# Kernel optimization log

Hardware: AMD Instinct MI355X
Metric: run time of the kernel (lower is better)

## Reference

```python
import jax, jax.numpy as jnp
import numpy as np

EMBED_DIM = 1024
NUM_HEADS = 16
HEAD_DIM = EMBED_DIM // NUM_HEADS


def setup_inputs() -> dict:
    key = jax.random.key(0)
    kx, kw1, kb1, kw2, kb2 = jax.random.split(key, 5)
    B, T, C = 4, 2048, EMBED_DIM
    s = 1.0 / np.sqrt(C)
    return {
        "x": jax.random.normal(kx, (B, T, C), dtype=jnp.float32),
        "qkv_w": jax.random.uniform(kw1, (3 * C, C), jnp.float32, -s, s),
        "qkv_b": jax.random.uniform(kb1, (3 * C,), jnp.float32, -s, s),
        "out_w": jax.random.uniform(kw2, (C, C), jnp.float32, -s, s),
        "out_b": jax.random.uniform(kb2, (C,), jnp.float32, -s, s),
    }


def reference(x, qkv_w, qkv_b, out_w, out_b):
    B, T, C = x.shape
    H, D = NUM_HEADS, HEAD_DIM
    qkv = x @ qkv_w.T + qkv_b                      # [B,T,3C]
    qkv = qkv.reshape(B, T, 3, H, D)
    q = qkv[:, :, 0].transpose(0, 2, 1, 3)         # [B,H,T,D]
    k = qkv[:, :, 1].transpose(0, 2, 1, 3)
    v = qkv[:, :, 2].transpose(0, 2, 1, 3)
    att = jnp.einsum("bhqd,bhkd->bhqk", q, k) / jnp.sqrt(jnp.float32(D))
    causal = jnp.tril(jnp.ones((T, T), dtype=bool))
    att = jnp.where(causal, att, -jnp.inf)
    att = jax.nn.softmax(att, axis=-1)
    out = jnp.einsum("bhqk,bhkd->bhqd", att, v)    # [B,H,T,D]
    out = out.transpose(0, 2, 1, 3).reshape(B, T, C)
    return out @ out_w.T + out_b
```

## Files before the change

kernel.cpp:

```cpp
#include <hip/hip_runtime.h>
#include <stdint.h>

typedef _Float16 f16;
typedef _Float16 f16x4 __attribute__((ext_vector_type(4)));
typedef _Float16 f16x8 __attribute__((ext_vector_type(8)));
typedef float f32x4 __attribute__((ext_vector_type(4)));

#define LOG2E 1.44269504088896340736f

__device__ __forceinline__ f32x4 mfma_16x16x32(f16x8 a, f16x8 b, f32x4 c) {
    return __builtin_amdgcn_mfma_f32_16x16x32_f16(a, b, c, 0, 0, 0);
}

__device__ __forceinline__ void gload_lds16(const void* g, void* l) {
    __builtin_amdgcn_global_load_lds(
        (const __attribute__((address_space(1))) unsigned int*)g,
        (__attribute__((address_space(3))) unsigned int*)l, 16, 0, 0);
}

__global__ void cast_f32_f16(const float* __restrict__ src, f16* __restrict__ dst, int n4) {
    int i = blockIdx.x * 256 + threadIdx.x;
    if (i >= n4) return;
    float4 v = reinterpret_cast<const float4*>(src)[i];
    f16x4 o;
    o[0] = (f16)v.x; o[1] = (f16)v.y; o[2] = (f16)v.z; o[3] = (f16)v.w;
    reinterpret_cast<f16x4*>(dst)[i] = o;
}

template<int MODE>
__global__ __launch_bounds__(256, 2)
void gemm_tn(const f16* __restrict__ A, const f16* __restrict__ W,
             const float* __restrict__ bias, void* __restrict__ outp,
             int M, int N, int K)
{
    __shared__ __align__(16) f16 As[128 * 32];
    __shared__ __align__(16) f16 Bs[128 * 32];

    const int lane = threadIdx.x & 63;
    const int wave = threadIdx.x >> 6;
    const int l15 = lane & 15, l4 = lane >> 4;
    const int row0 = blockIdx.y * 128;
    const int col0 = blockIdx.x * 128;
    const int wr = wave >> 1, wc = wave & 1;

    f32x4 acc[4][4] = {};

    const int srow = lane >> 2;
    const int scol = (lane & 3) * 8;

    for (int k0 = 0; k0 < K; k0 += 32) {
        __syncthreads();
        #pragma unroll
        for (int it = 0; it < 2; ++it) {
            int chunk = it * 4 + wave;
            const f16* gA = A + (size_t)(row0 + chunk * 16 + srow) * K + k0 + scol;
            gload_lds16(gA, As + chunk * 512);
            const f16* gB = W + (size_t)(col0 + chunk * 16 + srow) * K + k0 + scol;
            gload_lds16(gB, Bs + chunk * 512);
        }
        __syncthreads();

        f16x8 af[4], bf[4];
        #pragma unroll
        for (int m = 0; m < 4; ++m)
            af[m] = *reinterpret_cast<const f16x8*>(As + (wr * 64 + m * 16 + l15) * 32 + l4 * 8);
        #pragma unroll
        for (int n = 0; n < 4; ++n)
            bf[n] = *reinterpret_cast<const f16x8*>(Bs + (wc * 64 + n * 16 + l15) * 32 + l4 * 8);
        #pragma unroll
        for (int m = 0; m < 4; ++m)
            #pragma unroll
            for (int n = 0; n < 4; ++n)
                acc[m][n] = mfma_16x16x32(af[m], bf[n], acc[m][n]);
    }

    if (MODE == 0) {
        f16* qb = (f16*)outp;
        const size_t HS = (size_t)64 * 2048 * 64;
        #pragma unroll
        for (int m = 0; m < 4; ++m) {
            int rbase = row0 + wr * 64 + m * 16 + l4 * 4;
            #pragma unroll
            for (int n = 0; n < 4; ++n) {
                int j = col0 + wc * 64 + n * 16 + l15;
                int which = j >> 10;
                int h = (j >> 6) & 15;
                int d = j & 63;
                float bj = bias[j];
                f16* base = qb + (size_t)which * HS;
                float scale = (which == 0) ? (0.125f * LOG2E) : 1.0f;
                #pragma unroll
                for (int r = 0; r < 4; ++r) {
                    int row = rbase + r;
                    int b = row >> 11, t = row & 2047;
                    size_t off = ((size_t)(b * 16 + h) * 2048 + t) * 64 + d;
                    base[off] = (f16)((acc[m][n][r] + bj) * scale);
                }
            }
        }
    } else {
        float* O = (float*)outp;
        #pragma unroll
        for (int m = 0; m < 4; ++m) {
            int rbase = row0 + wr * 64 + m * 16 + l4 * 4;
            #pragma unroll
            for (int n = 0; n < 4; ++n) {
                int j = col0 + wc * 64 + n * 16 + l15;
                float bj = bias[j];
                #pragma unroll
                for (int r = 0; r < 4; ++r)
                    O[(size_t)(rbase + r) * N + j] = acc[m][n][r] + bj;
            }
        }
    }
}

__global__ __launch_bounds__(256, 2)
void attn_kernel(const f16* __restrict__ qb, const f16* __restrict__ kb,
                 const f16* __restrict__ vb, f16* __restrict__ ob)
{
    __shared__ __align__(16) f16 Ks[64 * 64];
    __shared__ __align__(16) f16 Vs[64][72];
    __shared__ __align__(16) f16 Ps[4][16][72];

    const int bh = blockIdx.x;
    const int qblk = (int)gridDim.y - 1 - (int)blockIdx.y;
    const int lane = threadIdx.x & 63;
    const int wave = threadIdx.x >> 6;
    const int l15 = lane & 15, l4 = lane >> 4;
    const int q0 = qblk * 64;

    const f16* Qp = qb + ((size_t)bh * 2048 + q0 + wave * 16) * 64;
    f16x8 aq[2];
    aq[0] = *reinterpret_cast<const f16x8*>(Qp + l15 * 64 + l4 * 8);
    aq[1] = *reinterpret_cast<const f16x8*>(Qp + l15 * 64 + 32 + l4 * 8);

    float Mr = -1e30f, Lr = 0.0f;
    f32x4 oacc[4] = {};

    for (int kv0 = 0; kv0 <= q0; kv0 += 64) {
        __syncthreads();

        const f16* Kt = kb + ((size_t)bh * 2048 + kv0) * 64;
        #pragma unroll
        for (int it = 0; it < 2; ++it) {
            int c = it * 4 + wave;
            int p = c * 1024 + lane * 16;
            int krow = p >> 7;
            int col16 = (p >> 4) & 7;
            int s16 = col16 ^ (krow & 7);
            gload_lds16(Kt + krow * 64 + s16 * 8, Ks + c * 512);
        }
        const f16* Vt = vb + ((size_t)bh * 2048 + kv0) * 64;
        {
            const int d0 = wave * 16;
            #pragma unroll
            for (int it = 0; it < 2; ++it) {
                f16x8 v = *reinterpret_cast<const f16x8*>(Vt + lane * 64 + d0 + it * 8);
                #pragma unroll
                for (int e = 0; e < 8; ++e)
                    Vs[d0 + it * 8 + e][lane] = v[e];
            }
        }
        __syncthreads();

        const bool diag = (kv0 == q0);

        f32x4 s[4];
        #pragma unroll
        for (int n = 0; n < 4; ++n) {
            int key = n * 16 + l15;
            int cs = key & 7;
            f32x4 c = {};
            #pragma unroll
            for (int kc = 0; kc < 2; ++kc) {
                f16x8 kf = *reinterpret_cast<const f16x8*>(Ks + key * 64 + (((kc * 4 + l4) ^ cs) * 8));
                c = mfma_16x16x32(kf, aq[kc], c);
            }
            s[n] = c;
        }

        if (diag) {
            #pragma unroll
            for (int n = 0; n < 4; ++n)
                #pragma unroll
                for (int r = 0; r < 4; ++r)
                    if (n * 16 + l4 * 4 + r > wave * 16 + l15) s[n][r] = -1e30f;
        }

        float mx = -1e30f;
        #pragma unroll
        for (int n = 0; n < 4; ++n)
            #pragma unroll
            for (int r = 0; r < 4; ++r)
                mx = fmaxf(mx, s[n][r]);
        mx = fmaxf(mx, __shfl_xor(mx, 16));
        mx = fmaxf(mx, __shfl_xor(mx, 32));
        float nm = fmaxf(Mr, mx);
        float alpha = exp2f(Mr - nm);
        Mr = nm;

        float rs = 0.0f;
        #pragma unroll
        for (int n = 0; n < 4; ++n) {
            f16x4 pk;
            #pragma unroll
            for (int r = 0; r < 4; ++r) {
                float pv = exp2f(s[n][r] - nm);
                rs += pv;
                pk[r] = (f16)pv;
            }
            *reinterpret_cast<f16x4*>(&Ps[wave][l15][n * 16 + l4 * 4]) = pk;
        }
        rs += __shfl_xor(rs, 16);
        rs += __shfl_xor(rs, 32);
        Lr = Lr * alpha + rs;

        float ar[4];
        #pragma unroll
        for (int r = 0; r < 4; ++r) ar[r] = __shfl(alpha, l4 * 4 + r);
        #pragma unroll
        for (int dt = 0; dt < 4; ++dt) {
            oacc[dt][0] *= ar[0]; oacc[dt][1] *= ar[1];
            oacc[dt][2] *= ar[2]; oacc[dt][3] *= ar[3];
        }

        f16x8 pa0 = *reinterpret_cast<const f16x8*>(&Ps[wave][l15][l4 * 8]);
        f16x8 pa1 = *reinterpret_cast<const f16x8*>(&Ps[wave][l15][32 + l4 * 8]);
        #pragma unroll
        for (int dt = 0; dt < 4; ++dt) {
            int d = dt * 16 + l15;
            f16x8 v0 = *reinterpret_cast<const f16x8*>(&Vs[d][l4 * 8]);
            f16x8 v1 = *reinterpret_cast<const f16x8*>(&Vs[d][32 + l4 * 8]);
            oacc[dt] = mfma_16x16x32(pa0, v0, oacc[dt]);
            oacc[dt] = mfma_16x16x32(pa1, v1, oacc[dt]);
        }
    }

    float lr[4];
    #pragma unroll
    for (int r = 0; r < 4; ++r) lr[r] = __shfl(Lr, l4 * 4 + r);

    const int b = bh >> 4, h = bh & 15;
    f16* O = ob + ((size_t)b * 2048 + q0 + wave * 16) * 1024 + h * 64;
    #pragma unroll
    for (int dt = 0; dt < 4; ++dt) {
        int d = dt * 16 + l15;
        #pragma unroll
        for (int r = 0; r < 4; ++r)
            O[(size_t)(l4 * 4 + r) * 1024 + d] = (f16)(oacc[dt][r] / lr[r]);
    }
}

extern "C" void kernel_launch(void* const* d_in, const int* in_sizes, int n_in,
                              void* d_out, int out_size, void* d_ws, size_t ws_size,
                              hipStream_t stream)
{
    const float* x    = (const float*)d_in[0];
    const float* qkvw = (const float*)d_in[1];
    const float* qkvb = (const float*)d_in[2];
    const float* outw = (const float*)d_in[3];
    const float* outb = (const float*)d_in[4];
    float* out = (float*)d_out;

    f16* x_h    = (f16*)d_ws;
    f16* qkvw_h = x_h + (size_t)8192 * 1024;
    f16* outw_h = qkvw_h + (size_t)3072 * 1024;
    f16* q_buf  = outw_h + (size_t)1024 * 1024;
    f16* att_o  = q_buf + (size_t)3 * 8388608;

    cast_f32_f16<<<8192, 256, 0, stream>>>(x, x_h, 2097152);
    cast_f32_f16<<<3072, 256, 0, stream>>>(qkvw, qkvw_h, 786432);
    cast_f32_f16<<<1024, 256, 0, stream>>>(outw, outw_h, 262144);

    gemm_tn<0><<<dim3(24, 64), 256, 0, stream>>>(x_h, qkvw_h, qkvb, q_buf, 8192, 3072, 1024);
    attn_kernel<<<dim3(64, 32), 256, 0, stream>>>(q_buf, q_buf + 8388608, q_buf + 2 * 8388608, att_o);
    gemm_tn<1><<<dim3(8, 64), 256, 0, stream>>>(att_o, outw_h, outb, out, 8192, 1024, 1024);
}
```

Baseline: 202.2 us.

## Enlarge attention query tile, cache K/V fragments, remap GEMM workgroups across XCDs

The attention kernel now gives each block 128 queries (32 per wave, two 16-row groups), so each K/V tile loaded into LDS is reused twice as much. K and V fragments are held in registers for both groups, and MFMA sections are wrapped in s_setprio. Softmax probabilities are packed to f16 with cvt_pkrtz. The GEMM remaps workgroup IDs so consecutive tiles land on the same XCD for L2 locality, and attention launch bounds move to 3 waves/SIMD. The extra register pressure from the held fragments may conflict with the higher occupancy target, and the round-toward-zero conversion changes rounding slightly.

```diff
diff --git a/kernel.cpp b/kernel.cpp
--- a/kernel.cpp
+++ b/kernel.cpp
@@ -2,6 +2,7 @@
 #include <stdint.h>
 
 typedef _Float16 f16;
+typedef _Float16 f16x2 __attribute__((ext_vector_type(2)));
 typedef _Float16 f16x4 __attribute__((ext_vector_type(4)));
 typedef _Float16 f16x8 __attribute__((ext_vector_type(8)));
 typedef float f32x4 __attribute__((ext_vector_type(4)));
@@ -16,6 +17,10 @@
     __builtin_amdgcn_global_load_lds(
         (const __attribute__((address_space(1))) unsigned int*)g,
         (__attribute__((address_space(3))) unsigned int*)l, 16, 0, 0);
+}
+
+__device__ __forceinline__ f16x2 cvt_pk_f16(float a, float b) {
+    return __builtin_bit_cast(f16x2, __builtin_amdgcn_cvt_pkrtz(a, b));
 }
 
 __global__ void cast_f32_f16(const float* __restrict__ src, f16* __restrict__ dst, int n4) {
@@ -39,8 +44,13 @@
     const int lane = threadIdx.x & 63;
     const int wave = threadIdx.x >> 6;
     const int l15 = lane & 15, l4 = lane >> 4;
-    const int row0 = blockIdx.y * 128;
-    const int col0 = blockIdx.x * 128;
+
+    const int nwg = (int)(gridDim.x * gridDim.y);
+    int orig = (int)(blockIdx.y * gridDim.x + blockIdx.x);
+    int cpx = nwg >> 3;
+    int w = (orig & 7) * cpx + (orig >> 3);
+    const int row0 = (w / (int)gridDim.x) * 128;
+    const int col0 = (w % (int)gridDim.x) * 128;
     const int wr = wave >> 1, wc = wave & 1;
 
     f32x4 acc[4][4] = {};
@@ -115,7 +125,7 @@
     }
 }
 
-__global__ __launch_bounds__(256, 2)
+__global__ __launch_bounds__(256, 3)
 void attn_kernel(const f16* __restrict__ qb, const f16* __restrict__ kb,
                  const f16* __restrict__ vb, f16* __restrict__ ob)
 {
@@ -123,132 +133,155 @@
     __shared__ __align__(16) f16 Vs[64][72];
     __shared__ __align__(16) f16 Ps[4][16][72];
 
-    const int bh = blockIdx.x;
+    const int tid = (int)threadIdx.x;
+    const int bh = (int)blockIdx.x;
     const int qblk = (int)gridDim.y - 1 - (int)blockIdx.y;
-    const int lane = threadIdx.x & 63;
-    const int wave = threadIdx.x >> 6;
+    const int lane = tid & 63;
+    const int wave = tid >> 6;
     const int l15 = lane & 15, l4 = lane >> 4;
-    const int q0 = qblk * 64;
-
-    const f16* Qp = qb + ((size_t)bh * 2048 + q0 + wave * 16) * 64;
-    f16x8 aq[2];
-    aq[0] = *reinterpret_cast<const f16x8*>(Qp + l15 * 64 + l4 * 8);
-    aq[1] = *reinterpret_cast<const f16x8*>(Qp + l15 * 64 + 32 + l4 * 8);
-
-    float Mr = -1e30f, Lr = 0.0f;
-    f32x4 oacc[4] = {};
-
-    for (int kv0 = 0; kv0 <= q0; kv0 += 64) {
+    const int q0 = qblk * 128;
+    const int qw = q0 + wave * 32;
+
+    const f16* Qp = qb + ((size_t)bh * 2048 + qw) * 64;
+    f16x8 aq[2][2];
+    #pragma unroll
+    for (int g = 0; g < 2; ++g)
+        #pragma unroll
+        for (int kc = 0; kc < 2; ++kc)
+            aq[g][kc] = *reinterpret_cast<const f16x8*>(Qp + (g * 16 + l15) * 64 + kc * 32 + l4 * 8);
+
+    float Mr[2] = {-1e30f, -1e30f}, Lr[2] = {0.0f, 0.0f};
+    f32x4 oacc[2][4] = {};
+
+    const int ntiles = q0 / 64 + 2;
+
+    for (int t = 0; t < ntiles; ++t) {
+        const int kv0 = t * 64;
         __syncthreads();
 
         const f16* Kt = kb + ((size_t)bh * 2048 + kv0) * 64;
         #pragma unroll
         for (int it = 0; it < 2; ++it) {
-            int c = it * 4 + wave;
-            int p = c * 1024 + lane * 16;
-            int krow = p >> 7;
-            int col16 = (p >> 4) & 7;
-            int s16 = col16 ^ (krow & 7);
-            gload_lds16(Kt + krow * 64 + s16 * 8, Ks + c * 512);
+            int c = it * 256 + tid;
+            int krow = c >> 3;
+            int s16 = (c & 7) ^ (krow & 7);
+            gload_lds16(Kt + krow * 64 + s16 * 8, Ks + it * 2048 + wave * 512);
         }
         const f16* Vt = vb + ((size_t)bh * 2048 + kv0) * 64;
-        {
-            const int d0 = wave * 16;
-            #pragma unroll
-            for (int it = 0; it < 2; ++it) {
-                f16x8 v = *reinterpret_cast<const f16x8*>(Vt + lane * 64 + d0 + it * 8);
-                #pragma unroll
-                for (int e = 0; e < 8; ++e)
-                    Vs[d0 + it * 8 + e][lane] = v[e];
-            }
+        #pragma unroll
+        for (int it = 0; it < 2; ++it) {
+            int dblk = wave * 2 + it;
+            f16x8 v = *reinterpret_cast<const f16x8*>(Vt + lane * 64 + dblk * 8);
+            #pragma unroll
+            for (int e = 0; e < 8; ++e)
+                Vs[dblk * 8 + e][lane] = v[e];
         }
         __syncthreads();
 
-        const bool diag = (kv0 == q0);
-
-        f32x4 s[4];
+        f16x8 kf[4][2], vf[4][2];
         #pragma unroll
         for (int n = 0; n < 4; ++n) {
             int key = n * 16 + l15;
-            int cs = key & 7;
-            f32x4 c = {};
-            #pragma unroll
-            for (int kc = 0; kc < 2; ++kc) {
-                f16x8 kf = *reinterpret_cast<const f16x8*>(Ks + key * 64 + (((kc * 4 + l4) ^ cs) * 8));
-                c = mfma_16x16x32(kf, aq[kc], c);
-            }
-            s[n] = c;
-        }
-
-        if (diag) {
+            #pragma unroll
+            for (int kc = 0; kc < 2; ++kc)
+                kf[n][kc] = *reinterpret_cast<const f16x8*>(Ks + key * 64 + (((kc * 4 + l4) ^ (key & 7)) * 8));
+        }
+        #pragma unroll
+        for (int dt = 0; dt < 4; ++dt) {
+            int d = dt * 16 + l15;
+            #pragma unroll
+            for (int kc = 0; kc < 2; ++kc)
+                vf[dt][kc] = *reinterpret_cast<const f16x8*>(&Vs[d][kc * 32 + l4 * 8]);
+        }
+
+        #pragma unroll
+        for (int g = 0; g < 2; ++g) {
+            const int qbase = qw + g * 16;
+            if (kv0 > qbase + 15) continue;
+
+            f32x4 s[4];
+            __builtin_amdgcn_s_setprio(1);
+            #pragma unroll
+            for (int n = 0; n < 4; ++n) {
+                f32x4 c = {};
+                c = mfma_16x16x32(kf[n][0], aq[g][0], c);
+                c = mfma_16x16x32(kf[n][1], aq[g][1], c);
+                s[n] = c;
+            }
+            __builtin_amdgcn_s_setprio(0);
+
+            if (kv0 + 63 > qbase) {
+                #pragma unroll
+                for (int n = 0; n < 4; ++n)
+                    #pragma unroll
+                    for (int r = 0; r < 4; ++r)
+                        if (kv0 + n * 16 + l4 * 4 + r > qbase + l15) s[n][r] = -1e30f;
+            }
+
+            float mx = -1e30f;
             #pragma unroll
             for (int n = 0; n < 4; ++n)
                 #pragma unroll
                 for (int r = 0; r < 4; ++r)
-                    if (n * 16 + l4 * 4 + r > wave * 16 + l15) s[n][r] = -1e30f;
-        }
-
-        float mx = -1e30f;
-        #pragma unroll
-        for (int n = 0; n < 4; ++n)
-            #pragma unroll
-            for (int r = 0; r < 4; ++r)
-                mx = fmaxf(mx, s[n][r]);
-        mx = fmaxf(mx, __shfl_xor(mx, 16));
-        mx = fmaxf(mx, __shfl_xor(mx, 32));
-        float nm = fmaxf(Mr, mx);
-        float alpha = exp2f(Mr - nm);
-        Mr = nm;
-
-        float rs = 0.0f;
-        #pragma unroll
-        for (int n = 0; n < 4; ++n) {
-            f16x4 pk;
-            #pragma unroll
-            for (int r = 0; r < 4; ++r) {
-                float pv = exp2f(s[n][r] - nm);
-                rs += pv;
-                pk[r] = (f16)pv;
-            }
-            *reinterpret_cast<f16x4*>(&Ps[wave][l15][n * 16 + l4 * 4]) = pk;
-        }
-        rs += __shfl_xor(rs, 16);
-        rs += __shfl_xor(rs, 32);
-        Lr = Lr * alpha + rs;
-
-        float ar[4];
-        #pragma unroll
-        for (int r = 0; r < 4; ++r) ar[r] = __shfl(alpha, l4 * 4 + r);
-        #pragma unroll
-        for (int dt = 0; dt < 4; ++dt) {
-            oacc[dt][0] *= ar[0]; oacc[dt][1] *= ar[1];
-            oacc[dt][2] *= ar[2]; oacc[dt][3] *= ar[3];
-        }
-
-        f16x8 pa0 = *reinterpret_cast<const f16x8*>(&Ps[wave][l15][l4 * 8]);
-        f16x8 pa1 = *reinterpret_cast<const f16x8*>(&Ps[wave][l15][32 + l4 * 8]);
+                    mx = fmaxf(mx, s[n][r]);
+            mx = fmaxf(mx, __shfl_xor(mx, 16));
+            mx = fmaxf(mx, __shfl_xor(mx, 32));
+            float nm = fmaxf(Mr[g], mx);
+            float alpha = exp2f(Mr[g] - nm);
+            Mr[g] = nm;
+
+            float rs = 0.0f;
+            #pragma unroll
+            for (int n = 0; n < 4; ++n) {
+                float p0 = exp2f(s[n][0] - nm);
+                float p1 = exp2f(s[n][1] - nm);
+                float p2 = exp2f(s[n][2] - nm);
+                float p3 = exp2f(s[n][3] - nm);
+                rs += (p0 + p1) + (p2 + p3);
+                f16x2 lo = cvt_pk_f16(p0, p1);
+                f16x2 hi = cvt_pk_f16(p2, p3);
+                f16x4 pk; pk[0] = lo[0]; pk[1] = lo[1]; pk[2] = hi[0]; pk[3] = hi[1];
+                *reinterpret_cast<f16x4*>(&Ps[wave][l15][n * 16 + l4 * 4]) = pk;
+            }
+            rs += __shfl_xor(rs, 16);
+            rs += __shfl_xor(rs, 32);
+            Lr[g] = Lr[g] * alpha + rs;
+
+            float ar[4];
+            #pragma unroll
+            for (int r = 0; r < 4; ++r) ar[r] = __shfl(alpha, l4 * 4 + r);
+            #pragma unroll
+            for (int dt = 0; dt < 4; ++dt) {
+                oacc[g][dt][0] *= ar[0]; oacc[g][dt][1] *= ar[1];
+                oacc[g][dt][2] *= ar[2]; oacc[g][dt][3] *= ar[3];
+            }
+
+            f16x8 pa0 = *reinterpret_cast<const f16x8*>(&Ps[wave][l15][l4 * 8]);
+            f16x8 pa1 = *reinterpret_cast<const f16x8*>(&Ps[wave][l15][32 + l4 * 8]);
+            __builtin_amdgcn_s_setprio(1);
+            #pragma unroll
+            for (int dt = 0; dt < 4; ++dt) {
+                oacc[g][dt] = mfma_16x16x32(pa0, vf[dt][0], oacc[g][dt]);
+                oacc[g][dt] = mfma_16x16x32(pa1, vf[dt][1], oacc[g][dt]);
+            }
+            __builtin_amdgcn_s_setprio(0);
+        }
+    }
+
+    const int b = bh >> 4, h = bh & 15;
+    #pragma unroll
+    for (int g = 0; g < 2; ++g) {
+        float lr[4];
+        #pragma unroll
+        for (int r = 0; r < 4; ++r) lr[r] = __shfl(Lr[g], l4 * 4 + r);
+        f16* O = ob + ((size_t)b * 2048 + qw + g * 16) * 1024 + h * 64;
         #pragma unroll
         for (int dt = 0; dt < 4; ++dt) {
             int d = dt * 16 + l15;
-            f16x8 v0 = *reinterpret_cast<const f16x8*>(&Vs[d][l4 * 8]);
-            f16x8 v1 = *reinterpret_cast<const f16x8*>(&Vs[d][32 + l4 * 8]);
-            oacc[dt] = mfma_16x16x32(pa0, v0, oacc[dt]);
-            oacc[dt] = mfma_16x16x32(pa1, v1, oacc[dt]);
-        }
-    }
-
-    float lr[4];
-    #pragma unroll
-    for (int r = 0; r < 4; ++r) lr[r] = __shfl(Lr, l4 * 4 + r);
-
-    const int b = bh >> 4, h = bh & 15;
-    f16* O = ob + ((size_t)b * 2048 + q0 + wave * 16) * 1024 + h * 64;
-    #pragma unroll
-    for (int dt = 0; dt < 4; ++dt) {
-        int d = dt * 16 + l15;
-        #pragma unroll
-        for (int r = 0; r < 4; ++r)
-            O[(size_t)(l4 * 4 + r) * 1024 + d] = (f16)(oacc[dt][r] / lr[r]);
+            #pragma unroll
+            for (int r = 0; r < 4; ++r)
+                O[(size_t)(l4 * 4 + r) * 1024 + d] = (f16)(oacc[g][dt][r] / lr[r]);
+        }
     }
 }
 
@@ -274,6 +307,6 @@
     cast_f32_f16<<<1024, 256, 0, stream>>>(outw, outw_h, 262144);
 
     gemm_tn<0><<<dim3(24, 64), 256, 0, stream>>>(x_h, qkvw_h, qkvb, q_buf, 8192, 3072, 1024);
-    attn_kernel<<<dim3(64, 32), 256, 0, stream>>>(q_buf, q_buf + 8388608, q_buf + 2 * 8388608, att_o);
+    attn_kernel<<<dim3(64, 16), 256, 0, stream>>>(q_buf, q_buf + 8388608, q_buf + 2 * 8388608, att_o);
     gemm_tn<1><<<dim3(8, 64), 256, 0, stream>>>(att_o, outw_h, outb, out, 8192, 1024, 1024);
 }
```

After: 197.4 us. -2.4%, faster.

## Double-buffer attention K/V tiles, add lazy rescale and XCD-aware GEMM tile remap

Applied to the files above, without the earlier changes.

The attention kernel now double-buffers K and V in LDS, prefetching the next tile's K with global-to-LDS loads and V into registers while the current tile computes, so only one barrier is needed per iteration. It also skips the online-softmax rescale unless the running max grows by more than a threshold, uses packed f16 conversion, raises MFMA wave priority, and bumps launch_bounds occupancy to 3. Separately, the GEMM remaps workgroup IDs so neighbouring tiles land on the same XCD for better L2 reuse. The costs are higher LDS use per block and reliance on the bounded-growth threshold for the accuracy of exp values.

```diff
diff --git a/kernel.cpp b/kernel.cpp
--- a/kernel.cpp
+++ b/kernel.cpp
@@ -2,6 +2,7 @@
 #include <stdint.h>
 
 typedef _Float16 f16;
+typedef _Float16 f16x2 __attribute__((ext_vector_type(2)));
 typedef _Float16 f16x4 __attribute__((ext_vector_type(4)));
 typedef _Float16 f16x8 __attribute__((ext_vector_type(8)));
 typedef float f32x4 __attribute__((ext_vector_type(4)));
@@ -16,6 +17,10 @@
     __builtin_amdgcn_global_load_lds(
         (const __attribute__((address_space(1))) unsigned int*)g,
         (__attribute__((address_space(3))) unsigned int*)l, 16, 0, 0);
+}
+
+__device__ __forceinline__ f16x2 cvt_pk_f16(float a, float b) {
+    return __builtin_bit_cast(f16x2, __builtin_amdgcn_cvt_pkrtz(a, b));
 }
 
 __global__ void cast_f32_f16(const float* __restrict__ src, f16* __restrict__ dst, int n4) {
@@ -39,8 +44,13 @@
     const int lane = threadIdx.x & 63;
     const int wave = threadIdx.x >> 6;
     const int l15 = lane & 15, l4 = lane >> 4;
-    const int row0 = blockIdx.y * 128;
-    const int col0 = blockIdx.x * 128;
+
+    const int nwg = (int)(gridDim.x * gridDim.y);
+    int orig = (int)(blockIdx.y * gridDim.x + blockIdx.x);
+    int cpx = nwg >> 3;
+    int w = (orig & 7) * cpx + (orig >> 3);
+    const int row0 = (w / (int)gridDim.x) * 128;
+    const int col0 = (w % (int)gridDim.x) * 128;
     const int wr = wave >> 1, wc = wave & 1;
 
     f32x4 acc[4][4] = {};
@@ -115,72 +125,92 @@
     }
 }
 
-__global__ __launch_bounds__(256, 2)
+__global__ __launch_bounds__(256, 3)
 void attn_kernel(const f16* __restrict__ qb, const f16* __restrict__ kb,
                  const f16* __restrict__ vb, f16* __restrict__ ob)
 {
-    __shared__ __align__(16) f16 Ks[64 * 64];
-    __shared__ __align__(16) f16 Vs[64][72];
+    __shared__ __align__(16) f16 Ks[2][64 * 64];
+    __shared__ __align__(16) f16 Vs[2][64][72];
     __shared__ __align__(16) f16 Ps[4][16][72];
 
-    const int bh = blockIdx.x;
+    const int tid = (int)threadIdx.x;
+    const int bh = (int)blockIdx.x;
     const int qblk = (int)gridDim.y - 1 - (int)blockIdx.y;
-    const int lane = threadIdx.x & 63;
-    const int wave = threadIdx.x >> 6;
+    const int lane = tid & 63;
+    const int wave = tid >> 6;
     const int l15 = lane & 15, l4 = lane >> 4;
     const int q0 = qblk * 64;
-
-    const f16* Qp = qb + ((size_t)bh * 2048 + q0 + wave * 16) * 64;
-    f16x8 aq[2];
-    aq[0] = *reinterpret_cast<const f16x8*>(Qp + l15 * 64 + l4 * 8);
-    aq[1] = *reinterpret_cast<const f16x8*>(Qp + l15 * 64 + 32 + l4 * 8);
+    const int qw = q0 + wave * 16;
+
+    const f16* Qp = qb + ((size_t)bh * 2048 + qw) * 64;
+    f16x8 aq0 = *reinterpret_cast<const f16x8*>(Qp + l15 * 64 + l4 * 8);
+    f16x8 aq1 = *reinterpret_cast<const f16x8*>(Qp + l15 * 64 + 32 + l4 * 8);
 
     float Mr = -1e30f, Lr = 0.0f;
     f32x4 oacc[4] = {};
 
-    for (int kv0 = 0; kv0 <= q0; kv0 += 64) {
+    const int ntiles = q0 / 64 + 1;
+    const f16* Kbh = kb + (size_t)bh * 2048 * 64;
+    const f16* Vbh = vb + (size_t)bh * 2048 * 64;
+
+    f16x8 vld0, vld1;
+    {
+        #pragma unroll
+        for (int it = 0; it < 2; ++it) {
+            int c = it * 256 + tid;
+            int krow = c >> 3;
+            int s16 = (c & 7) ^ (krow & 7);
+            gload_lds16(Kbh + krow * 64 + s16 * 8, &Ks[0][0] + it * 2048 + wave * 512);
+        }
+        vld0 = *reinterpret_cast<const f16x8*>(Vbh + lane * 64 + (wave * 2 + 0) * 8);
+        vld1 = *reinterpret_cast<const f16x8*>(Vbh + lane * 64 + (wave * 2 + 1) * 8);
+    }
+
+    for (int t = 0; t < ntiles; ++t) {
+        const int cur = t & 1;
+
+        #pragma unroll
+        for (int it = 0; it < 2; ++it) {
+            int dblk = wave * 2 + it;
+            const f16x8 v = it ? vld1 : vld0;
+            #pragma unroll
+            for (int e = 0; e < 8; ++e)
+                Vs[cur][dblk * 8 + e][lane] = v[e];
+        }
+
         __syncthreads();
 
-        const f16* Kt = kb + ((size_t)bh * 2048 + kv0) * 64;
-        #pragma unroll
-        for (int it = 0; it < 2; ++it) {
-            int c = it * 4 + wave;
-            int p = c * 1024 + lane * 16;
-            int krow = p >> 7;
-            int col16 = (p >> 4) & 7;
-            int s16 = col16 ^ (krow & 7);
-            gload_lds16(Kt + krow * 64 + s16 * 8, Ks + c * 512);
-        }
-        const f16* Vt = vb + ((size_t)bh * 2048 + kv0) * 64;
         {
-            const int d0 = wave * 16;
+            const int kvn = (t + 1 < ntiles) ? (t + 1) * 64 : t * 64;
+            const f16* Ktn = Kbh + (size_t)kvn * 64;
             #pragma unroll
             for (int it = 0; it < 2; ++it) {
-                f16x8 v = *reinterpret_cast<const f16x8*>(Vt + lane * 64 + d0 + it * 8);
-                #pragma unroll
-                for (int e = 0; e < 8; ++e)
-                    Vs[d0 + it * 8 + e][lane] = v[e];
+                int c = it * 256 + tid;
+                int krow = c >> 3;
+                int s16 = (c & 7) ^ (krow & 7);
+                gload_lds16(Ktn + krow * 64 + s16 * 8, &Ks[cur ^ 1][0] + it * 2048 + wave * 512);
             }
-        }
-        __syncthreads();
-
-        const bool diag = (kv0 == q0);
+            const f16* Vtn = Vbh + (size_t)kvn * 64;
+            vld0 = *reinterpret_cast<const f16x8*>(Vtn + lane * 64 + (wave * 2 + 0) * 8);
+            vld1 = *reinterpret_cast<const f16x8*>(Vtn + lane * 64 + (wave * 2 + 1) * 8);
+        }
 
         f32x4 s[4];
+        __builtin_amdgcn_s_setprio(1);
         #pragma unroll
         for (int n = 0; n < 4; ++n) {
             int key = n * 16 + l15;
             int cs = key & 7;
+            f16x8 kf0 = *reinterpret_cast<const f16x8*>(&Ks[cur][0] + key * 64 + ((l4 ^ cs) * 8));
+            f16x8 kf1 = *reinterpret_cast<const f16x8*>(&Ks[cur][0] + key * 64 + (((4 + l4) ^ cs) * 8));
             f32x4 c = {};
-            #pragma unroll
-            for (int kc = 0; kc < 2; ++kc) {
-                f16x8 kf = *reinterpret_cast<const f16x8*>(Ks + key * 64 + (((kc * 4 + l4) ^ cs) * 8));
-                c = mfma_16x16x32(kf, aq[kc], c);
-            }
+            c = mfma_16x16x32(kf0, aq0, c);
+            c = mfma_16x16x32(kf1, aq1, c);
             s[n] = c;
         }
-
-        if (diag) {
+        __builtin_amdgcn_s_setprio(0);
+
+        if (t == ntiles - 1) {
             #pragma unroll
             for (int n = 0; n < 4; ++n)
                 #pragma unroll
@@ -196,45 +226,51 @@
                 mx = fmaxf(mx, s[n][r]);
         mx = fmaxf(mx, __shfl_xor(mx, 16));
         mx = fmaxf(mx, __shfl_xor(mx, 32));
-        float nm = fmaxf(Mr, mx);
-        float alpha = exp2f(Mr - nm);
-        Mr = nm;
+
+        if (__any(mx > Mr + 8.0f)) {
+            float nm = fmaxf(Mr, mx);
+            float alpha = exp2f(Mr - nm);
+            Mr = nm;
+            float ar[4];
+            #pragma unroll
+            for (int r = 0; r < 4; ++r) ar[r] = __shfl(alpha, l4 * 4 + r);
+            #pragma unroll
+            for (int dt = 0; dt < 4; ++dt) {
+                oacc[dt][0] *= ar[0]; oacc[dt][1] *= ar[1];
+                oacc[dt][2] *= ar[2]; oacc[dt][3] *= ar[3];
+            }
+            Lr *= alpha;
+        }
 
         float rs = 0.0f;
         #pragma unroll
         for (int n = 0; n < 4; ++n) {
-            f16x4 pk;
-            #pragma unroll
-            for (int r = 0; r < 4; ++r) {
-                float pv = exp2f(s[n][r] - nm);
-                rs += pv;
-                pk[r] = (f16)pv;
-            }
+            float p0 = exp2f(s[n][0] - Mr);
+            float p1 = exp2f(s[n][1] - Mr);
+            float p2 = exp2f(s[n][2] - Mr);
+            float p3 = exp2f(s[n][3] - Mr);
+            rs += (p0 + p1) + (p2 + p3);
+            f16x2 lo = cvt_pk_f16(p0, p1);
+            f16x2 hi = cvt_pk_f16(p2, p3);
+            f16x4 pk; pk[0] = lo[0]; pk[1] = lo[1]; pk[2] = hi[0]; pk[3] = hi[1];
             *reinterpret_cast<f16x4*>(&Ps[wave][l15][n * 16 + l4 * 4]) = pk;
         }
         rs += __shfl_xor(rs, 16);
         rs += __shfl_xor(rs, 32);
-        Lr = Lr * alpha + rs;
-
-        float ar[4];
-        #pragma unroll
-        for (int r = 0; r < 4; ++r) ar[r] = __shfl(alpha, l4 * 4 + r);
-        #pragma unroll
-        for (int dt = 0; dt < 4; ++dt) {
-            oacc[dt][0] *= ar[0]; oacc[dt][1] *= ar[1];
-            oacc[dt][2] *= ar[2]; oacc[dt][3] *= ar[3];
-        }
+        Lr += rs;
 
         f16x8 pa0 = *reinterpret_cast<const f16x8*>(&Ps[wave][l15][l4 * 8]);
         f16x8 pa1 = *reinterpret_cast<const f16x8*>(&Ps[wave][l15][32 + l4 * 8]);
+        __builtin_amdgcn_s_setprio(1);
         #pragma unroll
         for (int dt = 0; dt < 4; ++dt) {
             int d = dt * 16 + l15;
-            f16x8 v0 = *reinterpret_cast<const f16x8*>(&Vs[d][l4 * 8]);
-            f16x8 v1 = *reinterpret_cast<const f16x8*>(&Vs[d][32 + l4 * 8]);
+            f16x8 v0 = *reinterpret_cast<const f16x8*>(&Vs[cur][d][l4 * 8]);
+            f16x8 v1 = *reinterpret_cast<const f16x8*>(&Vs[cur][d][32 + l4 * 8]);
             oacc[dt] = mfma_16x16x32(pa0, v0, oacc[dt]);
             oacc[dt] = mfma_16x16x32(pa1, v1, oacc[dt]);
         }
+        __builtin_amdgcn_s_setprio(0);
     }
 
     float lr[4];
@@ -242,7 +278,7 @@
     for (int r = 0; r < 4; ++r) lr[r] = __shfl(Lr, l4 * 4 + r);
 
     const int b = bh >> 4, h = bh & 15;
-    f16* O = ob + ((size_t)b * 2048 + q0 + wave * 16) * 1024 + h * 64;
+    f16* O = ob + ((size_t)b * 2048 + qw) * 1024 + h * 64;
     #pragma unroll
     for (int dt = 0; dt < 4; ++dt) {
         int d = dt * 16 + l15;
```

Result: no change. 198.3 us (-1.9%).
